# Kernel tuning notes

Hardware: AMD Instinct MI355X
Metric: run time of the kernel (lower is better)

Reference implementation:

```python
import math
import jax, jax.numpy as jnp
import numpy as np

MAX_LEN = 1024

def _sinusoidal_pe(seq_len, d_model):
    pos = jnp.arange(seq_len, dtype=jnp.float32)[:, None]
    div = jnp.exp(jnp.arange(0, d_model, 2, dtype=jnp.float32) * (-math.log(10000.0) / d_model))
    ang = pos * div  # [S, D/2]
    pe = jnp.zeros((seq_len, d_model), dtype=jnp.float32)
    pe = pe.at[:, 0::2].set(jnp.sin(ang))
    pe = pe.at[:, 1::2].set(jnp.cos(ang))
    return pe

def setup_inputs() -> dict:
    key = jax.random.key(0)
    ks = jax.random.split(key, 4)
    B, S, D, H = 4, 1024, 1024, 16
    x = jax.random.normal(ks[0], (B, S, D), dtype=jnp.float32)
    gamma = jnp.ones((D,), dtype=jnp.float32)
    beta = jnp.zeros((D,), dtype=jnp.float32)
    w_pos = jax.random.normal(ks[1], (2 * D, D), dtype=jnp.float32) * (1.0 / math.sqrt(D))
    w_tok = jax.random.normal(ks[2], (3 * D, D), dtype=jnp.float32) * (1.0 / math.sqrt(D))
    bias_table = jax.random.normal(ks[3], (2 * MAX_LEN, H), dtype=jnp.float32) * 0.02
    return {"x": x, "gamma": gamma, "beta": beta, "w_pos": w_pos, "w_tok": w_tok, "bias_table": bias_table}

def reference(x, gamma, beta, w_pos, w_tok, bias_table):
    B, S, D = x.shape
    H = bias_table.shape[1]
    dh = D // H
    scale = 1.0 / math.sqrt(2 * dh)

    # untied positional scores (identical across batch)
    pe = _sinusoidal_pe(S, D)                      # [S, D]
    pos = pe @ w_pos.T                             # [S, 2D]
    pos_k, pos_q = pos[:, :D], pos[:, D:]
    pos_k = pos_k.reshape(S, H, dh)
    pos_q = pos_q.reshape(S, H, dh)
    pos_attn = jnp.einsum('qhd,khd->hqk', pos_q, pos_k)  # [H, S, S]

    # token scores
    mu = jnp.mean(x, axis=-1, keepdims=True)
    var = jnp.mean((x - mu) ** 2, axis=-1, keepdims=True)
    xn = (x - mu) / jnp.sqrt(var + 1e-5) * gamma + beta
    tok = xn @ w_tok.T                             # [B, S, 3D]
    tok_k, tok_q, tok_v = jnp.split(tok, 3, axis=-1)
    tok_k = tok_k.reshape(B, S, H, dh)
    tok_q = tok_q.reshape(B, S, H, dh)
    tok_v = tok_v.reshape(B, S, H, dh)
    tok_attn = jnp.einsum('bqhd,bkhd->bhqk', tok_q, tok_k)  # [B, H, S, S]

    attn = (tok_attn + pos_attn[None]) / scale

    # relative-position bias
    rel = jnp.arange(S)[None, :] - jnp.arange(S)[:, None] + MAX_LEN  # [S, S]
    bias = bias_table[rel]                         # [S, S, H]
    attn = attn + jnp.transpose(bias, (2, 0, 1))[None]

    attn = jax.nn.softmax(attn, axis=-1)
    out = jnp.einsum('bhqk,bkhd->bqhd', attn, tok_v)
    return out.reshape(B, S, D)
```

## Files before the change

### kernel.cpp

```cpp
#include <hip/hip_runtime.h>
#include <math.h>

#define SB 1024
#define DM 1024
#define BB 4
#define NH 16
#define DH 64
#define ML 1024

typedef __attribute__((ext_vector_type(8))) short short8;
typedef __attribute__((ext_vector_type(8))) _Float16 half8;
typedef __attribute__((ext_vector_type(4))) float f32x4;
typedef unsigned short u16;

__device__ __forceinline__ u16 f2bf(float x) {
  unsigned u = __float_as_uint(x);
  u += 0x7fffu + ((u >> 16) & 1u);
  return (u16)(u >> 16);
}
__device__ __forceinline__ float bf2f(u16 h) { return __uint_as_float((unsigned)h << 16); }

__device__ __forceinline__ void async16(void* lds, const void* g) {
  __builtin_amdgcn_global_load_lds(
      (const __attribute__((address_space(1))) unsigned*)g,
      (__attribute__((address_space(3))) unsigned*)lds, 16, 0, 0);
}


__device__ __forceinline__ void pack16_body(int rt, int t, const float* __restrict__ src,
    _Float16* __restrict__ dH, _Float16* __restrict__ dL, float scale) {
  int r16 = t >> 4, ks = t & 15;
  const float* sp = src + (size_t)(rt * 16 + r16) * 1024 + ks * 64;
  float v[64];
  #pragma unroll
  for (int i = 0; i < 16; ++i) {
    float4 f = *(const float4*)(sp + i * 4);
    v[i*4+0] = f.x; v[i*4+1] = f.y; v[i*4+2] = f.z; v[i*4+3] = f.w;
  }
  #pragma unroll
  for (int hf = 0; hf < 2; ++hf) {
    int kt = ks * 2 + hf;
    #pragma unroll
    for (int gg = 0; gg < 4; ++gg) {
      half8 hv, lv;
      #pragma unroll
      for (int j = 0; j < 8; ++j) {
        float x = v[hf * 32 + gg * 8 + j] * scale;
        _Float16 h = (_Float16)x;
        hv[j] = h;
        lv[j] = (_Float16)(x - (float)h);
      }
      size_t off = ((size_t)(rt * 32 + kt) * 64 + r16 + gg * 16) * 8;
      *(half8*)(dH + off) = hv;
      *(half8*)(dL + off) = lv;
    }
  }
}

__device__ __forceinline__ void pe_pack_body(int rt, int t,
    _Float16* __restrict__ dH, _Float16* __restrict__ dL) {
  int r16 = t >> 4, ks = t & 15;
  int p = rt * 16 + r16;
  float v[64];
  #pragma unroll
  for (int i = 0; i < 32; ++i) {
    int c0 = ks * 64 + 2 * i;
    float div = expf((float)c0 * (-9.210340371976184f / (float)DM));
    float ang = (float)p * div;
    v[2*i]   = sinf(ang);
    v[2*i+1] = cosf(ang);
  }
  #pragma unroll
  for (int hf = 0; hf < 2; ++hf) {
    int kt = ks * 2 + hf;
    #pragma unroll
    for (int gg = 0; gg < 4; ++gg) {
      half8 hv, lv;
      #pragma unroll
      for (int j = 0; j < 8; ++j) {
        float x = v[hf * 32 + gg * 8 + j];
        _Float16 h = (_Float16)x;
        hv[j] = h;
        lv[j] = (_Float16)(x - (float)h);
      }
      size_t off = ((size_t)(rt * 32 + kt) * 64 + r16 + gg * 16) * 8;
      *(half8*)(dH + off) = hv;
      *(half8*)(dL + off) = lv;
    }
  }
}

__device__ __forceinline__ void ln_pack_body(int rt, int t, const float* __restrict__ x,
    const float* __restrict__ gamma, const float* __restrict__ beta,
    _Float16* __restrict__ dH, _Float16* __restrict__ dL) {
  int r16 = t >> 4, ks = t & 15;
  const float* sp = x + (size_t)(rt * 16 + r16) * 1024 + ks * 64;
  float v[64];
  float s1 = 0.f, s2 = 0.f;
  #pragma unroll
  for (int i = 0; i < 16; ++i) {
    float4 f = *(const float4*)(sp + i * 4);
    v[i*4+0] = f.x; v[i*4+1] = f.y; v[i*4+2] = f.z; v[i*4+3] = f.w;
    s1 += f.x + f.y + f.z + f.w;
    s2 += f.x*f.x + f.y*f.y + f.z*f.z + f.w*f.w;
  }
  #pragma unroll
  for (int off = 1; off < 16; off <<= 1) {
    s1 += __shfl_xor(s1, off, 64);
    s2 += __shfl_xor(s2, off, 64);
  }
  float mu = s1 * (1.0f / 1024.0f);
  float var = s2 * (1.0f / 1024.0f) - mu * mu;
  float rstd = rsqrtf(var + 1e-5f);
  #pragma unroll
  for (int hf = 0; hf < 2; ++hf) {
    int kt = ks * 2 + hf;
    #pragma unroll
    for (int gg = 0; gg < 4; ++gg) {
      const float* gp = gamma + ks * 64 + hf * 32 + gg * 8;
      const float* bp = beta  + ks * 64 + hf * 32 + gg * 8;
      half8 hv, lv;
      #pragma unroll
      for (int j = 0; j < 8; ++j) {
        float xn = (v[hf * 32 + gg * 8 + j] - mu) * rstd * gp[j] + bp[j];
        _Float16 h = (_Float16)xn;
        hv[j] = h;
        lv[j] = (_Float16)(xn - (float)h);
      }
      size_t off = ((size_t)(rt * 32 + kt) * 64 + r16 + gg * 16) * 8;
      *(half8*)(dH + off) = hv;
      *(half8*)(dL + off) = lv;
    }
  }
}

__global__ __launch_bounds__(256) void prep_all(
    const float* __restrict__ x, const float* __restrict__ gamma,
    const float* __restrict__ beta,
    const float* __restrict__ w_pos, const float* __restrict__ w_tok,
    _Float16* __restrict__ peH, _Float16* __restrict__ peL,
    _Float16* __restrict__ xnH, _Float16* __restrict__ xnL,
    _Float16* __restrict__ wpH, _Float16* __restrict__ wpL,
    _Float16* __restrict__ wtH, _Float16* __restrict__ wtL) {
  int bid = blockIdx.x;
  int t = threadIdx.x;
  if (bid < 64)       pe_pack_body(bid, t, peH, peL);
  else if (bid < 320) ln_pack_body(bid - 64, t, x, gamma, beta, xnH, xnL);
  else if (bid < 448) pack16_body(bid - 320, t, w_pos, wpH, wpL, 32.0f);
  else                pack16_body(bid - 448, t, w_tok, wtH, wtL, 32.0f);
}

#define GBM 128
#define GBN 256

__global__ __launch_bounds__(256, 2) void gemm16p(
    const _Float16* __restrict__ AtH, const _Float16* __restrict__ AtL,
    const _Float16* __restrict__ ApH, const _Float16* __restrict__ ApL,
    const _Float16* __restrict__ BtH, const _Float16* __restrict__ BtL,
    const _Float16* __restrict__ BpH, const _Float16* __restrict__ BpL,
    u16* __restrict__ KtfH, u16* __restrict__ KtfL,
    u16* __restrict__ KpfH, u16* __restrict__ KpfL,
    u16* __restrict__ QH, u16* __restrict__ QL,
    u16* __restrict__ pQH, u16* __restrict__ pQL,
    u16* __restrict__ vF, float sK, float sQ, float sV) {
  __shared__ _Float16 L[32 * 512];
  int t = threadIdx.x;
  int wv = t >> 6, lane = t & 63;
  int wm = wv >> 1, wn = wv & 1;
  int r16 = lane & 15, g = lane >> 4;

  int phys = blockIdx.x;
  int bid = (phys & 7) * 56 + (phys >> 3);
  bool isPos = (bid >= 384);
  int idx = isPos ? bid - 384 : bid;
  int n0, m0;
  const _Float16 *AH, *AL, *BH, *BL;
  if (isPos) { n0 = (idx & 7) * 256;  m0 = (idx >> 3) * 128;
               AH = ApH; AL = ApL; BH = BpH; BL = BpL; }
  else       { n0 = (idx % 12) * 256; m0 = (idx / 12) * 128;
               AH = AtH; AL = AtL; BH = BtH; BL = BtL; }
  int mt0 = m0 >> 4, nt0 = n0 >> 4;
  bool split = isPos || (n0 < 2048);

  f32x4 acc[4][8];
  #pragma unroll
  for (int i = 0; i < 4; ++i)
    #pragma unroll
    for (int j = 0; j < 8; ++j) acc[i][j] = (f32x4){0.f, 0.f, 0.f, 0.f};

  for (int kt = 0; kt < 32; ++kt) {
    __syncthreads();
    #pragma unroll
    for (int rd = 0; rd < 8; ++rd) {
      int ci = rd * 4 + wv;
      bool isAlo = (ci < 16) && (ci & 1);
      if (!split && isAlo) continue;
      const _Float16* src;
      if (ci < 16) {
        int mt = ci >> 1, pl = ci & 1;
        const _Float16* P = pl ? AL : AH;
        src = P + ((size_t)((mt0 + mt) * 32 + kt) * 64 + lane) * 8;
      } else {
        int nt = ci - 16;
        src = BH + ((size_t)((nt0 + nt) * 32 + kt) * 64 + lane) * 8;
      }
      async16(&L[ci * 512], src);
    }
    half8 blo[8];
    if (split) {
      #pragma unroll
      for (int j = 0; j < 8; ++j) {
        int ntg = nt0 + wn * 8 + j;
        blo[j] = *(const half8*)(BL + ((size_t)(ntg * 32 + kt) * 64 + lane) * 8);
      }
    }
    __syncthreads();

    half8 ah[4], al[4];
    #pragma unroll
    for (int i = 0; i < 4; ++i)
      ah[i] = *(const half8*)&L[(((wm * 4 + i) * 2 + 0) * 512) + lane * 8];
    if (split) {
      #pragma unroll
      for (int i = 0; i < 4; ++i)
        al[i] = *(const half8*)&L[(((wm * 4 + i) * 2 + 1) * 512) + lane * 8];
    }
    #pragma unroll
    for (int j = 0; j < 8; ++j) {
      half8 bh = *(const half8*)&L[((16 + wn * 8 + j) * 512) + lane * 8];
      #pragma unroll
      for (int i = 0; i < 4; ++i) {
        acc[i][j] = __builtin_amdgcn_mfma_f32_16x16x32_f16(ah[i], bh, acc[i][j], 0, 0, 0);
        if (split) {
          acc[i][j] = __builtin_amdgcn_mfma_f32_16x16x32_f16(al[i], bh, acc[i][j], 0, 0, 0);
          acc[i][j] = __builtin_amdgcn_mfma_f32_16x16x32_f16(ah[i], blo[j], acc[i][j], 0, 0, 0);
        }
      }
    }
  }

  int band = n0 >> 10;
  u16* fKH = isPos ? KpfH : KtfH;
  u16* fKL = isPos ? KpfL : KtfL;
  u16* qHo = isPos ? pQH  : QH;
  u16* qLo = isPos ? pQL  : QL;
  if (band == 1) {
    #pragma unroll
    for (int i = 0; i < 4; ++i)
      #pragma unroll
      for (int j = 0; j < 8; ++j) {
        int lc = (n0 & 1023) + wn * 128 + j * 16 + r16;
        #pragma unroll
        for (int reg = 0; reg < 4; ++reg) {
          int row = m0 + wm * 64 + i * 16 + g * 4 + reg;
          float cv = acc[i][j][reg] * sQ;
          u16 hi = f2bf(cv);
          qHo[(size_t)row * 1024 + lc] = hi;
          qLo[(size_t)row * 1024 + lc] = f2bf(cv - bf2f(hi));
        }
      }
  } else if (band == 0) {
    #pragma unroll
    for (int i = 0; i < 4; ++i)
      #pragma unroll
      for (int j = 0; j < 8; ++j) {
        int colg = n0 + wn * 128 + j * 16 + r16;
        int h = colg >> 6, dc = colg & 63;
        #pragma unroll
        for (int reg = 0; reg < 4; ++reg) {
          int row = m0 + wm * 64 + i * 16 + g * 4 + reg;
          int bhK = (row >> 10) * NH + h;
          size_t a = ((size_t)((bhK * 64 + ((row & 1023) >> 4)) * 2 + (dc >> 5)) << 9)
                   + ((row & 15) + 16 * ((dc >> 3) & 3)) * 8 + (dc & 7);
          float cv = acc[i][j][reg] * sK;
          u16 hi = f2bf(cv);
          fKH[a] = hi;
          fKL[a] = f2bf(cv - bf2f(hi));
        }
      }
  } else {
    #pragma unroll
    for (int i = 0; i < 4; ++i)
      #pragma unroll
      for (int j = 0; j < 8; ++j) {
        int colg = (n0 & 1023) + wn * 128 + j * 16 + r16;
        int h = colg >> 6, dc = colg & 63;
        #pragma unroll
        for (int reg = 0; reg < 4; ++reg) {
          int row = m0 + wm * 64 + i * 16 + g * 4 + reg;
          int s = row & 1023;
          size_t a = ((size_t)((((row >> 10) * NH + h) * 32 + (s >> 5)) * 4 + (dc >> 4)) << 9)
                   + ((s >> 3) & 3) * 128 + (s & 7) + (dc & 15) * 8;
          vF[a] = f2bf(acc[i][j][reg] * sV);
        }
      }
  }
}

__global__ __launch_bounds__(256, 2) void gemm16m(
    const _Float16* __restrict__ AtH, const _Float16* __restrict__ AtL,
    const _Float16* __restrict__ ApH, const _Float16* __restrict__ ApL,
    const float* __restrict__ Wt, const float* __restrict__ Wp,
    u16* __restrict__ KtfH, u16* __restrict__ KtfL,
    u16* __restrict__ KpfH, u16* __restrict__ KpfL,
    u16* __restrict__ QH, u16* __restrict__ QL,
    u16* __restrict__ pQH, u16* __restrict__ pQL,
    u16* __restrict__ vF, float sK, float sQ, float sV) {
  __shared__ _Float16 L[48 * 512];
  int t = threadIdx.x;
  int wv = t >> 6, lane = t & 63;
  int wm = wv >> 1, wn = wv & 1;
  int r16 = lane & 15, g = lane >> 4;

  int phys = blockIdx.x;
  int bid = (phys & 7) * 56 + (phys >> 3);
  bool isPos = (bid >= 384);
  int idx = isPos ? bid - 384 : bid;
  int n0, m0;
  const _Float16 *AH, *AL;
  const float* W;
  if (isPos) { n0 = (idx & 7) * 256;  m0 = (idx >> 3) * 128; AH = ApH; AL = ApL; W = Wp; }
  else       { n0 = (idx % 12) * 256; m0 = (idx / 12) * 128; AH = AtH; AL = AtL; W = Wt; }
  int mt0 = m0 >> 4, nt0 = n0 >> 4;
  bool split = isPos || (n0 < 2048);

  f32x4 acc[4][8];
  #pragma unroll
  for (int i = 0; i < 4; ++i)
    #pragma unroll
    for (int j = 0; j < 8; ++j) acc[i][j] = (f32x4){0.f, 0.f, 0.f, 0.f};

  for (int kt = 0; kt < 32; ++kt) {
    __syncthreads();
    #pragma unroll
    for (int rd = 0; rd < 4; ++rd) {
      int ci = rd * 4 + wv;
      int mt = ci >> 1, pl = ci & 1;
      if (!split && pl) continue;
      const _Float16* src = (pl ? AL : AH)
          + ((size_t)((mt0 + mt) * 32 + kt) * 64 + lane) * 8;
      async16(&L[ci * 512], src);
    }
    #pragma unroll
    for (int tt = 0; tt < 4; ++tt) {
      int nt = wv * 4 + tt;
      const float* wsrc = W + (size_t)((nt0 + nt) * 16 + r16) * 1024 + kt * 32 + g * 8;
      float4 w0 = *(const float4*)wsrc;
      float4 w1 = *(const float4*)(wsrc + 4);
      float wvv[8] = {w0.x, w0.y, w0.z, w0.w, w1.x, w1.y, w1.z, w1.w};
      half8 hv, lv;
      #pragma unroll
      for (int j = 0; j < 8; ++j) {
        float xx = wvv[j] * 32.0f;
        _Float16 h = (_Float16)xx;
        hv[j] = h;
        lv[j] = (_Float16)(xx - (float)h);
      }
      *(half8*)&L[(16 + nt) * 512 + lane * 8] = hv;
      if (split) *(half8*)&L[(32 + nt) * 512 + lane * 8] = lv;
    }
    __syncthreads();

    half8 ah[4], al[4];
    #pragma unroll
    for (int i = 0; i < 4; ++i)
      ah[i] = *(const half8*)&L[(((wm * 4 + i) * 2 + 0) * 512) + lane * 8];
    if (split) {
      #pragma unroll
      for (int i = 0; i < 4; ++i)
        al[i] = *(const half8*)&L[(((wm * 4 + i) * 2 + 1) * 512) + lane * 8];
    }
    #pragma unroll
    for (int j = 0; j < 8; ++j) {
      half8 bh = *(const half8*)&L[((16 + wn * 8 + j) * 512) + lane * 8];
      #pragma unroll
      for (int i = 0; i < 4; ++i) {
        acc[i][j] = __builtin_amdgcn_mfma_f32_16x16x32_f16(ah[i], bh, acc[i][j], 0, 0, 0);
        if (split) {
          half8 bl = *(const half8*)&L[((32 + wn * 8 + j) * 512) + lane * 8];
          acc[i][j] = __builtin_amdgcn_mfma_f32_16x16x32_f16(al[i], bh, acc[i][j], 0, 0, 0);
          acc[i][j] = __builtin_amdgcn_mfma_f32_16x16x32_f16(ah[i], bl, acc[i][j], 0, 0, 0);
        }
      }
    }
  }

  int band = n0 >> 10;
  u16* fKH = isPos ? KpfH : KtfH;
  u16* fKL = isPos ? KpfL : KtfL;
  u16* qHo = isPos ? pQH  : QH;
  u16* qLo = isPos ? pQL  : QL;
  if (band == 1) {
    #pragma unroll
    for (int i = 0; i < 4; ++i)
      #pragma unroll
      for (int j = 0; j < 8; ++j) {
        int lc = (n0 & 1023) + wn * 128 + j * 16 + r16;
        #pragma unroll
        for (int reg = 0; reg < 4; ++reg) {
          int row = m0 + wm * 64 + i * 16 + g * 4 + reg;
          float cv = acc[i][j][reg] * sQ;
          u16 hi = f2bf(cv);
          qHo[(size_t)row * 1024 + lc] = hi;
          qLo[(size_t)row * 1024 + lc] = f2bf(cv - bf2f(hi));
        }
      }
  } else if (band == 0) {
    #pragma unroll
    for (int i = 0; i < 4; ++i)
      #pragma unroll
      for (int j = 0; j < 8; ++j) {
        int colg = n0 + wn * 128 + j * 16 + r16;
        int h = colg >> 6, dc = colg & 63;
        #pragma unroll
        for (int reg = 0; reg < 4; ++reg) {
          int row = m0 + wm * 64 + i * 16 + g * 4 + reg;
          int bhK = (row >> 10) * NH + h;
          size_t a = ((size_t)((bhK * 64 + ((row & 1023) >> 4)) * 2 + (dc >> 5)) << 9)
                   + ((row & 15) + 16 * ((dc >> 3) & 3)) * 8 + (dc & 7);
          float cv = acc[i][j][reg] * sK;
          u16 hi = f2bf(cv);
          fKH[a] = hi;
          fKL[a] = f2bf(cv - bf2f(hi));
        }
      }
  } else {
    #pragma unroll
    for (int i = 0; i < 4; ++i)
      #pragma unroll
      for (int j = 0; j < 8; ++j) {
        int colg = (n0 & 1023) + wn * 128 + j * 16 + r16;
        int h = colg >> 6, dc = colg & 63;
        #pragma unroll
        for (int reg = 0; reg < 4; ++reg) {
          int row = m0 + wm * 64 + i * 16 + g * 4 + reg;
          int s = row & 1023;
          size_t a = ((size_t)((((row >> 10) * NH + h) * 32 + (s >> 5)) * 4 + (dc >> 4)) << 9)
                   + ((s >> 3) & 3) * 128 + (s & 7) + (dc & 15) * 8;
          vF[a] = f2bf(acc[i][j][reg] * sV);
        }
      }
  }
}

__global__ __launch_bounds__(256, 2) void attn_mfma10(
    const u16* __restrict__ KtfH, const u16* __restrict__ KtfL,
    const u16* __restrict__ KpfH, const u16* __restrict__ KpfL,
    const u16* __restrict__ QHg, const u16* __restrict__ QLg,
    const u16* __restrict__ pQH, const u16* __restrict__ pQL,
    const u16* __restrict__ Vf,
    const float* __restrict__ bt,
    float* __restrict__ out) {
  __shared__ u16 Klds[5 * 4096];
  __shared__ float biasL[2 * ML];
  __shared__ u16 Pb[4][16 * 72];

  int phys = blockIdx.x;
  int bid = (phys & 7) * 64 + (phys >> 3);
  int qt = bid & 7;
  int bh = bid >> 3;
  int b = bh >> 4, h = bh & 15;
  int q0 = qt * 128;
  int t = threadIdx.x;
  int wv = t >> 6, lane = t & 63;
  int g = lane >> 4, r16 = lane & 15;
  int lo = lane * 8;

  #pragma unroll
  for (int k = 0; k < 8; ++k)
    biasL[t + k * 256] = bt[(size_t)(t + k * 256) * NH + h];

  short8 qhi[2][4], qlo[2][4];
  #pragma unroll
  for (int cc = 0; cc < 2; ++cc) {
    int qrow = q0 + wv * 32 + cc * 16 + r16;
    #pragma unroll
    for (int c = 0; c < 4; ++c) {
      if (c < 2) {
        size_t off = (size_t)(b * SB + qrow) * 1024 + h * DH + c * 32 + g * 8;
        qhi[cc][c] = *(const short8*)(QHg + off);
        qlo[cc][c] = *(const short8*)(QLg + off);
      } else {
        size_t off = (size_t)qrow * 1024 + h * DH + (c - 2) * 32 + g * 8;
        qhi[cc][c] = *(const short8*)(pQH + off);
        qlo[cc][c] = *(const short8*)(pQL + off);
      }
    }
  }

  f32x4 O[2][4];
  #pragma unroll
  for (int cc = 0; cc < 2; ++cc)
    #pragma unroll
    for (int dt = 0; dt < 4; ++dt) O[cc][dt] = (f32x4){0.f, 0.f, 0.f, 0.f};
  float m_run[2][4], l_run[2][4];
  #pragma unroll
  for (int cc = 0; cc < 2; ++cc)
    #pragma unroll
    for (int reg = 0; reg < 4; ++reg) { m_run[cc][reg] = -3e38f; l_run[cc][reg] = 0.f; }

  int qb0 = q0 + wv * 32 + g * 4;
  const u16* ktHb = KtfH + (size_t)(bh * 64) * 1024;
  const u16* ktLb = KtfL + (size_t)(bh * 64) * 1024;
  const u16* kpHb = KpfH + (size_t)(h * 64) * 1024;
  const u16* kpLb = KpfL + (size_t)(h * 64) * 1024;
  const u16* vb   = Vf   + (size_t)(bh * 32) * 2048;
  int bb = ML + r16 - qb0;

  for (int ktr = 0; ktr < 16; ++ktr) {
    __syncthreads();

    {
      int p0 = wv * 512, p1 = (wv + 4) * 512;
      async16(&Klds[0 * 4096 + p0], ktHb + p0 + lo);
      async16(&Klds[0 * 4096 + p1], ktHb + p1 + lo);
      async16(&Klds[1 * 4096 + p0], ktLb + p0 + lo);
      async16(&Klds[1 * 4096 + p1], ktLb + p1 + lo);
      async16(&Klds[2 * 4096 + p0], kpHb + p0 + lo);
      async16(&Klds[2 * 4096 + p1], kpHb + p1 + lo);
      async16(&Klds[3 * 4096 + p0], kpLb + p0 + lo);
      async16(&Klds[3 * 4096 + p1], kpLb + p1 + lo);
      async16(&Klds[4 * 4096 + p0], vb + p0 + lo);
      async16(&Klds[4 * 4096 + p1], vb + p1 + lo);
    }

    float bias[2][4][4];
    #pragma unroll
    for (int nt = 0; nt < 4; ++nt)
      #pragma unroll
      for (int reg = 0; reg < 4; ++reg) {
        bias[0][nt][reg] = biasL[bb + nt * 16 - reg];
        bias[1][nt][reg] = biasL[bb - 16 + nt * 16 - reg];
      }

    asm volatile("s_waitcnt vmcnt(0)" ::: "memory");
    __syncthreads();

    f32x4 S[2][4];
    #pragma unroll
    for (int nt = 0; nt < 4; ++nt) {
      f32x4 a0 = (f32x4){0.f, 0.f, 0.f, 0.f};
      f32x4 a1 = (f32x4){0.f, 0.f, 0.f, 0.f};
      #pragma unroll
      for (int c = 0; c < 4; ++c) {
        int ch = (c < 2) ? 0 : 2;
        int co = c & 1;
        short8 bhi = *(const short8*)&Klds[(ch + 0) * 4096 + nt * 1024 + co * 512 + lo];
        short8 blo = *(const short8*)&Klds[(ch + 1) * 4096 + nt * 1024 + co * 512 + lo];
        a0 = __builtin_amdgcn_mfma_f32_16x16x32_bf16(qhi[0][c], bhi, a0, 0, 0, 0);
        a1 = __builtin_amdgcn_mfma_f32_16x16x32_bf16(qhi[1][c], bhi, a1, 0, 0, 0);
        a0 = __builtin_amdgcn_mfma_f32_16x16x32_bf16(qlo[0][c], bhi, a0, 0, 0, 0);
        a1 = __builtin_amdgcn_mfma_f32_16x16x32_bf16(qlo[1][c], bhi, a1, 0, 0, 0);
        a0 = __builtin_amdgcn_mfma_f32_16x16x32_bf16(qhi[0][c], blo, a0, 0, 0, 0);
        a1 = __builtin_amdgcn_mfma_f32_16x16x32_bf16(qhi[1][c], blo, a1, 0, 0, 0);
      }
      S[0][nt] = a0; S[1][nt] = a1;
    }

    short8 vfrag[2][4];
    #pragma unroll
    for (int kc = 0; kc < 2; ++kc)
      #pragma unroll
      for (int dt = 0; dt < 4; ++dt)
        vfrag[kc][dt] = *(const short8*)&Klds[4 * 4096 + (kc * 4 + dt) * 512 + lo];

    #pragma unroll
    for (int cc = 0; cc < 2; ++cc)
      #pragma unroll
      for (int nt = 0; nt < 4; ++nt)
        #pragma unroll
        for (int reg = 0; reg < 4; ++reg)
          S[cc][nt][reg] += bias[cc][nt][reg];

    float tm[2][4], al[2][4];
    #pragma unroll
    for (int cc = 0; cc < 2; ++cc)
      #pragma unroll
      for (int reg = 0; reg < 4; ++reg)
        tm[cc][reg] = fmaxf(fmaxf(S[cc][0][reg], S[cc][1][reg]),
                            fmaxf(S[cc][2][reg], S[cc][3][reg]));
    #pragma unroll
    for (int off = 1; off < 16; off <<= 1)
      #pragma unroll
      for (int cc = 0; cc < 2; ++cc)
        #pragma unroll
        for (int reg = 0; reg < 4; ++reg)
          tm[cc][reg] = fmaxf(tm[cc][reg], __shfl_xor(tm[cc][reg], off, 64));
    #pragma unroll
    for (int cc = 0; cc < 2; ++cc)
      #pragma unroll
      for (int reg = 0; reg < 4; ++reg) {
        float mn = fmaxf(m_run[cc][reg], tm[cc][reg]);
        al[cc][reg] = __expf(m_run[cc][reg] - mn);
        m_run[cc][reg] = mn;
      }
    float ts[2][4] = {{0.f, 0.f, 0.f, 0.f}, {0.f, 0.f, 0.f, 0.f}};
    #pragma unroll
    for (int cc = 0; cc < 2; ++cc)
      #pragma unroll
      for (int nt = 0; nt < 4; ++nt)
        #pragma unroll
        for (int reg = 0; reg < 4; ++reg) {
          float p = __expf(S[cc][nt][reg] - m_run[cc][reg]);
          S[cc][nt][reg] = p;
          ts[cc][reg] += p;
        }
    #pragma unroll
    for (int cc = 0; cc < 2; ++cc)
      #pragma unroll
      for (int reg = 0; reg < 4; ++reg)
        l_run[cc][reg] = l_run[cc][reg] * al[cc][reg] + ts[cc][reg];
    #pragma unroll
    for (int cc = 0; cc < 2; ++cc)
      #pragma unroll
      for (int dt = 0; dt < 4; ++dt)
        #pragma unroll
        for (int reg = 0; reg < 4; ++reg)
          O[cc][dt][reg] *= al[cc][reg];

    #pragma unroll
    for (int cc = 0; cc < 2; ++cc) {
      u16* pb = Pb[wv];
      #pragma unroll
      for (int nt = 0; nt < 4; ++nt)
        #pragma unroll
        for (int reg = 0; reg < 4; ++reg)
          pb[(g * 4 + reg) * 72 + nt * 16 + r16] = f2bf(S[cc][nt][reg]);
      #pragma unroll
      for (int kc = 0; kc < 2; ++kc) {
        short8 pa = *(const short8*)&Pb[wv][r16 * 72 + kc * 32 + g * 8];
        #pragma unroll
        for (int dt = 0; dt < 4; ++dt)
          O[cc][dt] = __builtin_amdgcn_mfma_f32_16x16x32_bf16(pa, vfrag[kc][dt], O[cc][dt], 0, 0, 0);
      }
    }

    ktHb += 4096; ktLb += 4096; kpHb += 4096; kpLb += 4096;
    vb += 4096; bb += 64;
  }

  #pragma unroll
  for (int off = 1; off < 16; off <<= 1)
    #pragma unroll
    for (int cc = 0; cc < 2; ++cc)
      #pragma unroll
      for (int reg = 0; reg < 4; ++reg)
        l_run[cc][reg] += __shfl_xor(l_run[cc][reg], off, 64);
  #pragma unroll
  for (int cc = 0; cc < 2; ++cc)
    #pragma unroll
    for (int reg = 0; reg < 4; ++reg) l_run[cc][reg] = 1.0f / l_run[cc][reg];
  #pragma unroll
  for (int cc = 0; cc < 2; ++cc)
    #pragma unroll
    for (int dt = 0; dt < 4; ++dt)
      #pragma unroll
      for (int reg = 0; reg < 4; ++reg)
        out[(size_t)(b * SB + qb0 + cc * 16 + reg) * DM + h * DH + dt * 16 + r16] =
            O[cc][dt][reg] * l_run[cc][reg];
}

extern "C" void kernel_launch(void* const* d_in, const int* in_sizes, int n_in,
                              void* d_out, int out_size, void* d_ws, size_t ws_size,
                              hipStream_t stream) {
  const float* x     = (const float*)d_in[0];
  const float* gamma = (const float*)d_in[1];
  const float* beta  = (const float*)d_in[2];
  const float* w_pos = (const float*)d_in[3];
  const float* w_tok = (const float*)d_in[4];
  const float* bt    = (const float*)d_in[5];
  float* out = (float*)d_out;
  float* ws  = (float*)d_ws;
  const size_t M1 = 1u << 20;
  const float IS = 11.313708498984761f;

  u16 *KtfH, *KtfL, *KpfH, *KpfL, *QH, *QL, *posQH, *posQL, *Vf;

  if (ws_size >= 22 * M1 * 4) {
    _Float16* peH = (_Float16*)(ws);
    _Float16* peL = (_Float16*)(ws + M1 / 2);
    _Float16* xnH = (_Float16*)(ws + 1 * M1);
    _Float16* xnL = (_Float16*)(ws + 3 * M1);
    _Float16* wpH = (_Float16*)(ws + 5 * M1);
    _Float16* wpL = (_Float16*)(ws + 6 * M1);
    _Float16* wtH = (_Float16*)(ws + 7 * M1);
    _Float16* wtL = (_Float16*)(ws + 8 * M1 + M1/2);
    KpfH  = (u16*)(ws + 10 * M1);
    KpfL  = (u16*)(ws + 10 * M1 + M1 / 2);
    posQH = (u16*)(ws + 11 * M1);
    posQL = (u16*)(ws + 11 * M1 + M1 / 2);
    KtfH  = (u16*)(ws + 12 * M1);
    KtfL  = (u16*)(ws + 14 * M1);
    QH    = (u16*)(ws + 16 * M1);
    QL    = (u16*)(ws + 18 * M1);
    Vf    = (u16*)(ws + 20 * M1);

    prep_all<<<640, 256, 0, stream>>>(x, gamma, beta, w_pos, w_tok,
        peH, peL, xnH, xnL, wpH, wpL, wtH, wtL);
    gemm16p<<<448, 256, 0, stream>>>(
        xnH, xnL, peH, peL, wtH, wtL, wpH, wpL,
        KtfH, KtfL, KpfH, KpfL, QH, QL, posQH, posQL, Vf,
        1.0f / 32.0f, IS / 32.0f, 1.0f / 32.0f);
  } else {
    _Float16* peH = (_Float16*)(ws);
    _Float16* peL = (_Float16*)(ws + M1 / 2);
    _Float16* xnH = (_Float16*)(ws + 1 * M1);
    _Float16* xnL = (_Float16*)(ws + 3 * M1);
    KpfH  = (u16*)(ws + 5 * M1);
    KpfL  = (u16*)(ws + 5 * M1 + M1 / 2);
    posQH = (u16*)(ws + 6 * M1);
    posQL = (u16*)(ws + 6 * M1 + M1 / 2);
    KtfH  = (u16*)(ws + 7 * M1);
    KtfL  = (u16*)(ws + 9 * M1);
    QH    = (u16*)(ws + 11 * M1);
    QL    = (u16*)(ws + 13 * M1);
    Vf    = (u16*)(ws + 15 * M1);

    prep_all<<<320, 256, 0, stream>>>(x, gamma, beta, w_pos, w_tok,
        peH, peL, xnH, xnL, (_Float16*)nullptr, (_Float16*)nullptr,
        (_Float16*)nullptr, (_Float16*)nullptr);
    gemm16m<<<448, 256, 0, stream>>>(
        xnH, xnL, peH, peL, w_tok, w_pos,
        KtfH, KtfL, KpfH, KpfL, QH, QL, posQH, posQL, Vf,
        1.0f / 32.0f, IS / 32.0f, 1.0f / 32.0f);
  }

  attn_mfma10<<<BB * NH * (SB / 128), 256, 0, stream>>>(
      KtfH, KtfL, KpfH, KpfL, QH, QL, posQH, posQL, Vf, bt, out);
}
```

Before: 251.7 us.

## Prefetch next K/V tile in attention and double-buffer GEMM LDS staging

The attention kernel now issues the async global-to-LDS loads for the next key/value tile as soon as all waves have pulled the current K and V fragments into registers. Those loads then overlap with the bias add, softmax and P·V MFMAs instead of being exposed at the top of each iteration. The GEMM kernel gets a two-slot LDS buffer, with explicit vmcnt waits and raw barriers, so tile k+1 loads while tile k is computed. This doubles that kernel's shared memory. The visible host path launches gemm16m, so the gemm16p change may not run. The hand-placed waitcnt counts must match the number of outstanding loads exactly, or correctness can break.

```diff
diff --git a/kernel.cpp b/kernel.cpp
--- a/kernel.cpp
+++ b/kernel.cpp
@@ -12,6 +12,12 @@
 typedef __attribute__((ext_vector_type(8))) _Float16 half8;
 typedef __attribute__((ext_vector_type(4))) float f32x4;
 typedef unsigned short u16;
+
+#define S_BARRIER() __builtin_amdgcn_s_barrier()
+#define SCHED_FENCE() __builtin_amdgcn_sched_barrier(0)
+#define WAITV(N) asm volatile("s_waitcnt vmcnt(" #N ")" ::: "memory")
+#define WAITLGKM() asm volatile("s_waitcnt lgkmcnt(0)" ::: "memory")
+#define WAITVL() asm volatile("s_waitcnt vmcnt(0) lgkmcnt(0)" ::: "memory")
 
 __device__ __forceinline__ u16 f2bf(float x) {
   unsigned u = __float_as_uint(x);
@@ -150,8 +156,38 @@
   else                pack16_body(bid - 448, t, w_tok, wtH, wtL, 32.0f);
 }
 
-#define GBM 128
-#define GBN 256
+
+__device__ __forceinline__ void stage_gemm(bool split, int wv, int lane,
+    _Float16* Lb, const _Float16* AH, const _Float16* AL, const _Float16* BH,
+    int mt0, int nt0, int kt) {
+  if (split) {
+    #pragma unroll
+    for (int rd = 0; rd < 8; ++rd) {
+      int ci = rd * 4 + wv;
+      const _Float16* src;
+      if (ci < 16) {
+        int mt = ci >> 1, pl = ci & 1;
+        src = (pl ? AL : AH) + ((size_t)((mt0 + mt) * 32 + kt) * 64 + lane) * 8;
+      } else {
+        src = BH + ((size_t)((nt0 + ci - 16) * 32 + kt) * 64 + lane) * 8;
+      }
+      async16(&Lb[ci * 512], src);
+    }
+  } else {
+    #pragma unroll
+    for (int rd = 0; rd < 6; ++rd) {
+      int idx = wv * 6 + rd;
+      int ci = (idx < 8) ? (idx * 2) : (idx + 8);
+      const _Float16* src;
+      if (ci < 16) {
+        src = AH + ((size_t)((mt0 + (ci >> 1)) * 32 + kt) * 64 + lane) * 8;
+      } else {
+        src = BH + ((size_t)((nt0 + ci - 16) * 32 + kt) * 64 + lane) * 8;
+      }
+      async16(&Lb[ci * 512], src);
+    }
+  }
+}
 
 __global__ __launch_bounds__(256, 2) void gemm16p(
     const _Float16* __restrict__ AtH, const _Float16* __restrict__ AtL,
@@ -163,7 +199,7 @@
     u16* __restrict__ QH, u16* __restrict__ QL,
     u16* __restrict__ pQH, u16* __restrict__ pQL,
     u16* __restrict__ vF, float sK, float sQ, float sV) {
-  __shared__ _Float16 L[32 * 512];
+  __shared__ _Float16 L[2][32 * 512];
   int t = threadIdx.x;
   int wv = t >> 6, lane = t & 63;
   int wm = wv >> 1, wn = wv & 1;
@@ -188,24 +224,10 @@
     #pragma unroll
     for (int j = 0; j < 8; ++j) acc[i][j] = (f32x4){0.f, 0.f, 0.f, 0.f};
 
+  stage_gemm(split, wv, lane, &L[0][0], AH, AL, BH, mt0, nt0, 0);
+
   for (int kt = 0; kt < 32; ++kt) {
-    __syncthreads();
-    #pragma unroll
-    for (int rd = 0; rd < 8; ++rd) {
-      int ci = rd * 4 + wv;
-      bool isAlo = (ci < 16) && (ci & 1);
-      if (!split && isAlo) continue;
-      const _Float16* src;
-      if (ci < 16) {
-        int mt = ci >> 1, pl = ci & 1;
-        const _Float16* P = pl ? AL : AH;
-        src = P + ((size_t)((mt0 + mt) * 32 + kt) * 64 + lane) * 8;
-      } else {
-        int nt = ci - 16;
-        src = BH + ((size_t)((nt0 + nt) * 32 + kt) * 64 + lane) * 8;
-      }
-      async16(&L[ci * 512], src);
-    }
+    _Float16* Lc = &L[kt & 1][0];
     half8 blo[8];
     if (split) {
       #pragma unroll
@@ -214,20 +236,26 @@
         blo[j] = *(const half8*)(BL + ((size_t)(ntg * 32 + kt) * 64 + lane) * 8);
       }
     }
-    __syncthreads();
+    SCHED_FENCE();
+    if (kt < 31)
+      stage_gemm(split, wv, lane, &L[(kt + 1) & 1][0], AH, AL, BH, mt0, nt0, kt + 1);
+    if (split) { if (kt < 31) WAITV(16); else WAITV(8); }
+    else       { if (kt < 31) WAITV(6);  else WAITV(0); }
+    S_BARRIER();
+    SCHED_FENCE();
 
     half8 ah[4], al[4];
     #pragma unroll
     for (int i = 0; i < 4; ++i)
-      ah[i] = *(const half8*)&L[(((wm * 4 + i) * 2 + 0) * 512) + lane * 8];
+      ah[i] = *(const half8*)&Lc[(((wm * 4 + i) * 2 + 0) * 512) + lane * 8];
     if (split) {
       #pragma unroll
       for (int i = 0; i < 4; ++i)
-        al[i] = *(const half8*)&L[(((wm * 4 + i) * 2 + 1) * 512) + lane * 8];
+        al[i] = *(const half8*)&Lc[(((wm * 4 + i) * 2 + 1) * 512) + lane * 8];
     }
     #pragma unroll
     for (int j = 0; j < 8; ++j) {
-      half8 bh = *(const half8*)&L[((16 + wn * 8 + j) * 512) + lane * 8];
+      half8 bh = *(const half8*)&Lc[((16 + wn * 8 + j) * 512) + lane * 8];
       #pragma unroll
       for (int i = 0; i < 4; ++i) {
         acc[i][j] = __builtin_amdgcn_mfma_f32_16x16x32_f16(ah[i], bh, acc[i][j], 0, 0, 0);
@@ -237,6 +265,9 @@
         }
       }
     }
+    WAITLGKM();
+    S_BARRIER();
+    SCHED_FENCE();
   }
 
   int band = n0 >> 10;
@@ -443,7 +474,23 @@
   }
 }
 
-__global__ __launch_bounds__(256, 2) void attn_mfma10(
+__device__ __forceinline__ void stage_attn(u16* Klds,
+    const u16* ktH, const u16* ktL, const u16* kpH, const u16* kpL,
+    const u16* vb, int wv, int lo) {
+  int p0 = wv * 512, p1 = (wv + 4) * 512;
+  async16(&Klds[0 * 4096 + p0], ktH + p0 + lo);
+  async16(&Klds[0 * 4096 + p1], ktH + p1 + lo);
+  async16(&Klds[1 * 4096 + p0], ktL + p0 + lo);
+  async16(&Klds[1 * 4096 + p1], ktL + p1 + lo);
+  async16(&Klds[2 * 4096 + p0], kpH + p0 + lo);
+  async16(&Klds[2 * 4096 + p1], kpH + p1 + lo);
+  async16(&Klds[3 * 4096 + p0], kpL + p0 + lo);
+  async16(&Klds[3 * 4096 + p1], kpL + p1 + lo);
+  async16(&Klds[4 * 4096 + p0], vb + p0 + lo);
+  async16(&Klds[4 * 4096 + p1], vb + p1 + lo);
+}
+
+__global__ __launch_bounds__(256, 2) void attn_mfma11(
     const u16* __restrict__ KtfH, const u16* __restrict__ KtfL,
     const u16* __restrict__ KpfH, const u16* __restrict__ KpfL,
     const u16* __restrict__ QHg, const u16* __restrict__ QLg,
@@ -507,22 +554,12 @@
   const u16* vb   = Vf   + (size_t)(bh * 32) * 2048;
   int bb = ML + r16 - qb0;
 
+  stage_attn(Klds, ktHb, ktLb, kpHb, kpLb, vb, wv, lo);
+
   for (int ktr = 0; ktr < 16; ++ktr) {
-    __syncthreads();
-
-    {
-      int p0 = wv * 512, p1 = (wv + 4) * 512;
-      async16(&Klds[0 * 4096 + p0], ktHb + p0 + lo);
-      async16(&Klds[0 * 4096 + p1], ktHb + p1 + lo);
-      async16(&Klds[1 * 4096 + p0], ktLb + p0 + lo);
-      async16(&Klds[1 * 4096 + p1], ktLb + p1 + lo);
-      async16(&Klds[2 * 4096 + p0], kpHb + p0 + lo);
-      async16(&Klds[2 * 4096 + p1], kpHb + p1 + lo);
-      async16(&Klds[3 * 4096 + p0], kpLb + p0 + lo);
-      async16(&Klds[3 * 4096 + p1], kpLb + p1 + lo);
-      async16(&Klds[4 * 4096 + p0], vb + p0 + lo);
-      async16(&Klds[4 * 4096 + p1], vb + p1 + lo);
-    }
+    WAITVL();
+    S_BARRIER();
+    SCHED_FENCE();
 
     float bias[2][4][4];
     #pragma unroll
@@ -532,9 +569,6 @@
         bias[0][nt][reg] = biasL[bb + nt * 16 - reg];
         bias[1][nt][reg] = biasL[bb - 16 + nt * 16 - reg];
       }
-
-    asm volatile("s_waitcnt vmcnt(0)" ::: "memory");
-    __syncthreads();
 
     f32x4 S[2][4];
     #pragma unroll
@@ -564,6 +598,15 @@
       for (int dt = 0; dt < 4; ++dt)
         vfrag[kc][dt] = *(const short8*)&Klds[4 * 4096 + (kc * 4 + dt) * 512 + lo];
 
+    WAITLGKM();
+    S_BARRIER();
+    SCHED_FENCE();
+    if (ktr < 15) {
+      ktHb += 4096; ktLb += 4096; kpHb += 4096; kpLb += 4096; vb += 4096;
+      stage_attn(Klds, ktHb, ktLb, kpHb, kpLb, vb, wv, lo);
+    }
+    SCHED_FENCE();
+
     #pragma unroll
     for (int cc = 0; cc < 2; ++cc)
       #pragma unroll
@@ -635,8 +678,7 @@
       }
     }
 
-    ktHb += 4096; ktLb += 4096; kpHb += 4096; kpLb += 4096;
-    vb += 4096; bb += 64;
+    bb += 64;
   }
 
   #pragma unroll
@@ -725,6 +767,6 @@
         1.0f / 32.0f, IS / 32.0f, 1.0f / 32.0f);
   }
 
-  attn_mfma10<<<BB * NH * (SB / 128), 256, 0, stream>>>(
+  attn_mfma11<<<BB * NH * (SB / 128), 256, 0, stream>>>(
       KtfH, KtfL, KpfH, KpfL, QH, QL, posQH, posQL, Vf, bt, out);
 }
```

Measured after the change: 256.4 us. No clear change (+1.9%).
